# Optimization experiments

Hardware: AMD Instinct MI355X
Metric: run time of the kernel (lower is better)

## Reference

```python
import jax, jax.numpy as jnp
import numpy as np

K = 5          # kernel_size
PAD = 2        # padding
EPS = 1e-4     # epsilon (noise scale)
DEG = 4        # polynomial degree


def _unfold(x, k, pad):
    # PyTorch nn.Unfold ordering: feature index = c*k*k + i*k + j
    B, C, H, W = x.shape
    xp = jnp.pad(x, ((0, 0), (0, 0), (pad, pad), (pad, pad)))
    Ho = H + 2 * pad - k + 1
    Wo = W + 2 * pad - k + 1
    patches = jnp.stack(
        [xp[:, :, i:i + Ho, j:j + Wo] for i in range(k) for j in range(k)],
        axis=2,
    )  # [B, C, k*k, Ho, Wo]
    return patches.reshape(B, C * k * k, Ho * Wo), Ho, Wo


def setup_inputs() -> dict:
    key = jax.random.key(0)
    k1, k2, k3 = jax.random.split(key, 3)
    B, C, H = 4, 3, 96
    O, S = 32, 2
    y2 = jax.random.normal(k1, (B, C, H, H), dtype=jnp.float32)
    # kaiming_uniform_ on [O,C,k,k,S]: fan_in = C*k*k*S = 150
    bound = float(np.sqrt(6.0 / (C * K * K * S)))
    weights = jax.random.uniform(k2, (O, C, K, K, S), dtype=jnp.float32,
                                 minval=-bound, maxval=bound)
    L = H * H  # Ho*Wo with pad=2, k=5
    noise = jax.random.normal(k3, (B, C * K * K, L), dtype=jnp.float32)
    return {"y2": y2, "weights": weights, "noise": noise}


def reference(y2, weights, noise):
    O, C, k, _, S = weights.shape
    y, Ho, Wo = _unfold(y2, k, PAD)            # [B, n, L], n = C*k*k
    y = y + EPS * noise
    # normalize: torch.std default is unbiased (ddof=1) over feature dim
    std = jnp.std(y, axis=1, ddof=1)           # [B, L]
    y = y / std[:, None, :]

    X = weights.reshape(O, C * k * k, S)        # [O, n, S]
    # columns: [ones, X, X^2, ..., X^DEG]  -> P = 1 + S*DEG
    cols = [jnp.ones_like(X[:, :, :1])] + [X ** (i + 1) for i in range(DEG)]
    Xf = jnp.concatenate(cols, axis=2)          # [O, n, P]

    cov = jnp.einsum('onp,onq->opq', Xf, Xf)    # X^T X  [O, P, P]
    cov_inv = jnp.linalg.inv(cov)
    M = jnp.einsum('opq,onq->opn', cov_inv, Xf)
    W = jnp.einsum('opn,bnl->bopl', M, y)
    pred = jnp.einsum('onp,bopl->bonl', Xf, W)   # [B, O, n, L]

    err = jnp.mean((y[:, None, :, :] - pred) ** 2, axis=2)  # [B, O, L]
    err = err.reshape(err.shape[0], err.shape[1], Ho, Wo)

    e1 = np.exp(-1.0)
    A = (jnp.exp(-err) - e1) / (1.0 - e1)
    return A - 0.5
```

## Files before the change

### kernel.cpp

```cpp
#include <hip/hip_runtime.h>
#include <hip/hip_bf16.h>
#include <math.h>


typedef __attribute__((ext_vector_type(8))) short bf16x8;
typedef __attribute__((ext_vector_type(4))) float f32x4;
typedef __attribute__((ext_vector_type(4))) int i32x4;

#define TRI(p, q) ((p) * ((p) + 1) / 2 + (q))

__global__ __launch_bounds__(96) void srn_setup(const float* __restrict__ Wt,
                                                __hip_bfloat16* __restrict__ Gb) {
  const int o = blockIdx.x;
  __shared__ double Xf[96][9];
  __shared__ double Cm[9][9];
  __shared__ double Rf[45];
  __shared__ double scs[9];
  const int tid = threadIdx.x;
  if (tid < 75) {
    double x0 = (double)Wt[o * 150 + tid * 2 + 0];
    double x1 = (double)Wt[o * 150 + tid * 2 + 1];
    Xf[tid][0] = 1.0;
    double p = x0;
    Xf[tid][1] = p; p *= x0; Xf[tid][2] = p; p *= x0; Xf[tid][3] = p; p *= x0; Xf[tid][4] = p;
    p = x1;
    Xf[tid][5] = p; p *= x1; Xf[tid][6] = p; p *= x1; Xf[tid][7] = p; p *= x1; Xf[tid][8] = p;
  }
  __syncthreads();
  if (tid < 81) {
    const int p = tid / 9, q = tid - (tid / 9) * 9;
    double s = 0.0;
#pragma unroll
    for (int n = 0; n < 75; n++) s += Xf[n][p] * Xf[n][q];
    Cm[p][q] = s;
  }
  __syncthreads();
  if (tid == 0) {
    double sc[9];
#pragma unroll
    for (int p = 0; p < 9; p++) sc[p] = 1.0 / sqrt(Cm[p][p]);
    double A[45];
#pragma unroll
    for (int p = 0; p < 9; p++)
#pragma unroll
      for (int q = 0; q <= p; q++) A[TRI(p, q)] = Cm[p][q] * sc[p] * sc[q];
#pragma unroll
    for (int p = 0; p < 9; p++) {
      double s = A[TRI(p, p)];
#pragma unroll
      for (int i = 0; i < p; i++) s -= A[TRI(p, i)] * A[TRI(p, i)];
      const double rp = sqrt(s);
      A[TRI(p, p)] = rp;
      const double ir = 1.0 / rp;
#pragma unroll
      for (int r = p + 1; r < 9; r++) {
        double t = A[TRI(r, p)];
#pragma unroll
        for (int i = 0; i < p; i++) t -= A[TRI(r, i)] * A[TRI(p, i)];
        A[TRI(r, p)] = t * ir;
      }
    }
#pragma unroll
    for (int k = 0; k < 45; k++) Rf[k] = A[k];
#pragma unroll
    for (int p = 0; p < 9; p++) Rf[TRI(p, p)] = 1.0 / A[TRI(p, p)];
#pragma unroll
    for (int p = 0; p < 9; p++) scs[p] = sc[p];
  }
  __syncthreads();
  if (tid < 96) {
    double z[9];
    if (tid < 75) {
#pragma unroll
      for (int p = 0; p < 9; p++) {
        double s = scs[p] * Xf[tid][p];
#pragma unroll
        for (int i = 0; i < p; i++) s -= Rf[TRI(p, i)] * z[i];
        z[p] = s * Rf[TRI(p, p)];
      }
    } else {
#pragma unroll
      for (int p = 0; p < 9; p++) z[p] = 0.0;
    }
    const int t = o >> 1;
    const int ch = tid >> 5;
    const int g4r = (tid >> 3) & 3;
    const int j = tid & 7;
    const int base = ((t * 3 + ch) << 9) + ((o & 1) << 6) + (g4r << 7) + j;
#pragma unroll
    for (int p = 1; p < 9; p++)
      Gb[base + ((p - 1) << 3)] = __float2bfloat16((float)z[p]);
  }
}

__global__ __launch_bounds__(512, 2) void srn_main(const float* __restrict__ y2,
                                                   const __hip_bfloat16* __restrict__ Gbh,
                                                   float* __restrict__ out) {
  __shared__ __attribute__((aligned(16))) short Gs[24576];
  __shared__ int tab[96];

  const int tid = threadIdx.x;

  if (tid < 96) {
    const int c = (tid * 41) >> 10;
    const int r = tid - c * 25;
    const int di = (r * 52) >> 8;
    const int dj = r - di * 5;
    tab[tid] = (di << 20) | (dj << 16) | (c * 9216 + di * 96 + dj);
  }

  {
    const i32x4* gsrc = (const i32x4*)Gbh;
    i32x4* gdst = (i32x4*)Gs;
#pragma unroll
    for (int k = 0; k < 6; k++) gdst[k * 512 + tid] = gsrc[k * 512 + tid];
  }
  __syncthreads();

  const int lane = tid & 63;
  const int wv = tid >> 6;
  const int m16 = lane & 15, g4 = lane >> 4;
  const int tau2 = blockIdx.x * 8 + wv;
  const int b = tau2 / 576;
  const int rem = tau2 - b * 576;
  const int h = rem / 6;
  const int w0 = (rem - h * 6) * 16;
  const int w = w0 + m16;
  const int l = h * 96 + w;

  i32x4 e[6];
  const i32x4* tb = (const i32x4*)tab;
#pragma unroll
  for (int ch = 0; ch < 3; ch++) {
    e[ch * 2 + 0] = tb[ch * 8 + g4 * 2 + 0];
    e[ch * 2 + 1] = tb[ch * 8 + g4 * 2 + 1];
  }

  const float* yb = y2 + b * 27648;
  const bool fast = ((unsigned)(h - 2) < 92u) && (w0 >= 16) && (w0 <= 64);
  const int live1 = 11 - g4 * 8;
  float vv[24];
  if (fast) {
    const float* yl = yb + (l - 194);
#pragma unroll
    for (int ch = 0; ch < 3; ch++)
#pragma unroll
      for (int j = 0; j < 8; j++) {
        const int ent = (j < 4) ? e[ch * 2][j] : e[ch * 2 + 1][j - 4];
        float v = 0.f;
        if (ch < 2 || j < live1) v = yl[ent & 0xFFFF];
        vv[ch * 8 + j] = v;
      }
  } else {
#pragma unroll
    for (int ch = 0; ch < 3; ch++)
#pragma unroll
      for (int j = 0; j < 8; j++) {
        const int ent = (j < 4) ? e[ch * 2][j] : e[ch * 2 + 1][j - 4];
        float v = 0.f;
        if (ch < 2 || j < live1) {
          const int di = ent >> 20, dj = (ent >> 16) & 15;
          const int off = ent & 0xFFFF;
          const int c9216 = off - di * 96 - dj;
          const int hh = h + di - 2, ww = w + dj - 2;
          const float m = (((unsigned)hh < 96u) && ((unsigned)ww < 96u)) ? 1.f : 0.f;
          v = yb[c9216 + min(max(hh, 0), 95) * 96 + min(max(ww, 0), 95)] * m;
        }
        vv[ch * 8 + j] = v;
      }
  }

  bf16x8 Bf[3];
  float up = 0.f, sp = 0.f;
#pragma unroll
  for (int ch = 0; ch < 3; ch++)
#pragma unroll
    for (int j = 0; j < 8; j++) {
      const __hip_bfloat16 hb = __float2bfloat16(vv[ch * 8 + j]);
      const float vr = __bfloat162float(hb);
      sp += vr;
      up = fmaf(vr, vr, up);
      Bf[ch][j] = *reinterpret_cast<const short*>(&hb);
    }
  up += __shfl_xor(up, 16); up += __shfl_xor(up, 32);
  sp += __shfl_xor(sp, 16); sp += __shfl_xor(sp, 32);

  const float qbase = sp * sp * (1.f / 75.f);
  const float var = (up - qbase) * (1.f / 74.f);
  const float cerr = 1.f / (75.f * var);
  const float e1 = 0.36787944117144233f;
  const float r1 = 1.f / (1.f - e1);
  const float c2 = e1 * r1 + 0.5f;

  const short* Ab = Gs + lane * 8;
  float* ob = out + b * 294912 + l;
  const f32x4 z = {0.f, 0.f, 0.f, 0.f};
#pragma unroll
  for (int t = 0; t < 16; t++) {
    const short* At = Ab + t * 1536;
    const bf16x8 A0 = *(const bf16x8*)(At);
    const bf16x8 A1 = *(const bf16x8*)(At + 512);
    const bf16x8 A2 = *(const bf16x8*)(At + 1024);
    f32x4 acc = z;
    acc = __builtin_amdgcn_mfma_f32_16x16x32_bf16(A0, Bf[0], acc, 0, 0, 0);
    acc = __builtin_amdgcn_mfma_f32_16x16x32_bf16(A1, Bf[1], acc, 0, 0, 0);
    acc = __builtin_amdgcn_mfma_f32_16x16x32_bf16(A2, Bf[2], acc, 0, 0, 0);
    float qp = acc[0] * acc[0];
    qp = fmaf(acc[1], acc[1], qp);
    qp = fmaf(acc[2], acc[2], qp);
    qp = fmaf(acc[3], acc[3], qp);
    qp += __shfl_xor(qp, 16);
    const float q = qp + qbase;
    const float err = (up - q) * cerr;
    const float a = fmaf(__expf(-err), r1, -c2);
    if ((g4 & 1) == 0) ob[(2 * t + (g4 >> 1)) * 9216] = a;
  }
}

extern "C" void kernel_launch(void* const* d_in, const int* in_sizes, int n_in,
                              void* d_out, int out_size, void* d_ws, size_t ws_size,
                              hipStream_t stream) {
  const float* y2 = (const float*)d_in[0];
  const float* Wt = (const float*)d_in[1];
  float* out = (float*)d_out;
  __hip_bfloat16* Gb = (__hip_bfloat16*)d_ws;

  srn_setup<<<32, 96, 0, stream>>>(Wt, Gb);
  srn_main<<<288, 512, 0, stream>>>(y2, Gb, out);
}
```

Baseline: 20.86 us.

## Fuse weight-regression setup into main kernel, recomputing Cholesky per block

Removes the separate setup kernel and the workspace round-trip. Every block of the main kernel now computes the 32 Gram matrices, their Cholesky factors and the projected bf16 operand itself, using 16-lane shuffle reductions, and writes the result straight into shared memory. This saves one kernel launch and the dependent global write/read. In exchange, each of the 288 blocks repeats the double-precision setup work, and register pressure rises because of 45-element double arrays per thread.

```diff
diff --git a/kernel.cpp b/kernel.cpp
--- a/kernel.cpp
+++ b/kernel.cpp
@@ -9,94 +9,11 @@
 
 #define TRI(p, q) ((p) * ((p) + 1) / 2 + (q))
 
-__global__ __launch_bounds__(96) void srn_setup(const float* __restrict__ Wt,
-                                                __hip_bfloat16* __restrict__ Gb) {
-  const int o = blockIdx.x;
-  __shared__ double Xf[96][9];
-  __shared__ double Cm[9][9];
-  __shared__ double Rf[45];
-  __shared__ double scs[9];
-  const int tid = threadIdx.x;
-  if (tid < 75) {
-    double x0 = (double)Wt[o * 150 + tid * 2 + 0];
-    double x1 = (double)Wt[o * 150 + tid * 2 + 1];
-    Xf[tid][0] = 1.0;
-    double p = x0;
-    Xf[tid][1] = p; p *= x0; Xf[tid][2] = p; p *= x0; Xf[tid][3] = p; p *= x0; Xf[tid][4] = p;
-    p = x1;
-    Xf[tid][5] = p; p *= x1; Xf[tid][6] = p; p *= x1; Xf[tid][7] = p; p *= x1; Xf[tid][8] = p;
-  }
-  __syncthreads();
-  if (tid < 81) {
-    const int p = tid / 9, q = tid - (tid / 9) * 9;
-    double s = 0.0;
-#pragma unroll
-    for (int n = 0; n < 75; n++) s += Xf[n][p] * Xf[n][q];
-    Cm[p][q] = s;
-  }
-  __syncthreads();
-  if (tid == 0) {
-    double sc[9];
-#pragma unroll
-    for (int p = 0; p < 9; p++) sc[p] = 1.0 / sqrt(Cm[p][p]);
-    double A[45];
-#pragma unroll
-    for (int p = 0; p < 9; p++)
-#pragma unroll
-      for (int q = 0; q <= p; q++) A[TRI(p, q)] = Cm[p][q] * sc[p] * sc[q];
-#pragma unroll
-    for (int p = 0; p < 9; p++) {
-      double s = A[TRI(p, p)];
-#pragma unroll
-      for (int i = 0; i < p; i++) s -= A[TRI(p, i)] * A[TRI(p, i)];
-      const double rp = sqrt(s);
-      A[TRI(p, p)] = rp;
-      const double ir = 1.0 / rp;
-#pragma unroll
-      for (int r = p + 1; r < 9; r++) {
-        double t = A[TRI(r, p)];
-#pragma unroll
-        for (int i = 0; i < p; i++) t -= A[TRI(r, i)] * A[TRI(p, i)];
-        A[TRI(r, p)] = t * ir;
-      }
-    }
-#pragma unroll
-    for (int k = 0; k < 45; k++) Rf[k] = A[k];
-#pragma unroll
-    for (int p = 0; p < 9; p++) Rf[TRI(p, p)] = 1.0 / A[TRI(p, p)];
-#pragma unroll
-    for (int p = 0; p < 9; p++) scs[p] = sc[p];
-  }
-  __syncthreads();
-  if (tid < 96) {
-    double z[9];
-    if (tid < 75) {
-#pragma unroll
-      for (int p = 0; p < 9; p++) {
-        double s = scs[p] * Xf[tid][p];
-#pragma unroll
-        for (int i = 0; i < p; i++) s -= Rf[TRI(p, i)] * z[i];
-        z[p] = s * Rf[TRI(p, p)];
-      }
-    } else {
-#pragma unroll
-      for (int p = 0; p < 9; p++) z[p] = 0.0;
-    }
-    const int t = o >> 1;
-    const int ch = tid >> 5;
-    const int g4r = (tid >> 3) & 3;
-    const int j = tid & 7;
-    const int base = ((t * 3 + ch) << 9) + ((o & 1) << 6) + (g4r << 7) + j;
-#pragma unroll
-    for (int p = 1; p < 9; p++)
-      Gb[base + ((p - 1) << 3)] = __float2bfloat16((float)z[p]);
-  }
-}
-
-__global__ __launch_bounds__(512, 2) void srn_main(const float* __restrict__ y2,
-                                                   const __hip_bfloat16* __restrict__ Gbh,
-                                                   float* __restrict__ out) {
+__global__ __launch_bounds__(512, 2) void srn_fused(const float* __restrict__ y2,
+                                                    const float* __restrict__ Wt,
+                                                    float* __restrict__ out) {
   __shared__ __attribute__((aligned(16))) short Gs[24576];
+  __shared__ double RfL[32][54];
   __shared__ int tab[96];
 
   const int tid = threadIdx.x;
@@ -109,11 +26,97 @@
     tab[tid] = (di << 20) | (dj << 16) | (c * 9216 + di * 96 + dj);
   }
 
-  {
-    const i32x4* gsrc = (const i32x4*)Gbh;
-    i32x4* gdst = (i32x4*)Gs;
-#pragma unroll
-    for (int k = 0; k < 6; k++) gdst[k * 512 + tid] = gsrc[k * 512 + tid];
+  const int og = tid >> 4;
+  const int oj = tid & 15;
+
+  double cv[45];
+#pragma unroll
+  for (int i = 0; i < 45; i++) cv[i] = 0.0;
+#pragma unroll
+  for (int r = 0; r < 5; r++) {
+    const int n = oj + 16 * r;
+    if (n < 75) {
+      const double x0 = (double)Wt[og * 150 + 2 * n];
+      const double x1 = (double)Wt[og * 150 + 2 * n + 1];
+      double xf[9];
+      xf[0] = 1.0;
+      xf[1] = x0; xf[2] = x0 * x0; xf[3] = xf[2] * x0; xf[4] = xf[2] * xf[2];
+      xf[5] = x1; xf[6] = x1 * x1; xf[7] = xf[6] * x1; xf[8] = xf[6] * xf[6];
+      int idx = 0;
+#pragma unroll
+      for (int p = 0; p < 9; p++)
+#pragma unroll
+        for (int q = 0; q <= p; q++, idx++) cv[idx] = fma(xf[p], xf[q], cv[idx]);
+    }
+  }
+#pragma unroll
+  for (int m = 1; m < 16; m <<= 1)
+#pragma unroll
+    for (int i = 0; i < 45; i++) cv[i] += __shfl_xor(cv[i], m);
+
+  if (oj == 0) {
+    double sc[9];
+#pragma unroll
+    for (int p = 0; p < 9; p++) sc[p] = 1.0 / sqrt(cv[TRI(p, p)]);
+    double A[45];
+#pragma unroll
+    for (int p = 0; p < 9; p++)
+#pragma unroll
+      for (int q = 0; q <= p; q++) A[TRI(p, q)] = cv[TRI(p, q)] * sc[p] * sc[q];
+#pragma unroll
+    for (int p = 0; p < 9; p++) {
+      double s = A[TRI(p, p)];
+#pragma unroll
+      for (int i = 0; i < p; i++) s -= A[TRI(p, i)] * A[TRI(p, i)];
+      const double rp = sqrt(s);
+      A[TRI(p, p)] = rp;
+      const double ir = 1.0 / rp;
+#pragma unroll
+      for (int r = p + 1; r < 9; r++) {
+        double t = A[TRI(r, p)];
+#pragma unroll
+        for (int i = 0; i < p; i++) t -= A[TRI(r, i)] * A[TRI(p, i)];
+        A[TRI(r, p)] = t * ir;
+      }
+    }
+#pragma unroll
+    for (int k = 0; k < 45; k++) RfL[og][k] = A[k];
+#pragma unroll
+    for (int p = 0; p < 9; p++) RfL[og][TRI(p, p)] = 1.0 / A[TRI(p, p)];
+#pragma unroll
+    for (int p = 0; p < 9; p++) RfL[og][45 + p] = sc[p];
+  }
+  __syncthreads();
+
+#pragma unroll
+  for (int k = 0; k < 6; k++) {
+    const int n = oj + 16 * k;
+    double z[9];
+    if (n < 75) {
+      const double x0 = (double)Wt[og * 150 + 2 * n];
+      const double x1 = (double)Wt[og * 150 + 2 * n + 1];
+      double xf[9];
+      xf[0] = 1.0;
+      xf[1] = x0; xf[2] = x0 * x0; xf[3] = xf[2] * x0; xf[4] = xf[2] * xf[2];
+      xf[5] = x1; xf[6] = x1 * x1; xf[7] = xf[6] * x1; xf[8] = xf[6] * xf[6];
+#pragma unroll
+      for (int p = 0; p < 9; p++) {
+        double s = RfL[og][45 + p] * xf[p];
+#pragma unroll
+        for (int i = 0; i < p; i++) s -= RfL[og][TRI(p, i)] * z[i];
+        z[p] = s * RfL[og][TRI(p, p)];
+      }
+    } else {
+#pragma unroll
+      for (int p = 0; p < 9; p++) z[p] = 0.0;
+    }
+    const int t = og >> 1, ch = n >> 5, g4r = (n >> 3) & 3, jj = n & 7;
+    const int base = ((t * 3 + ch) << 9) + ((og & 1) << 6) + (g4r << 7) + jj;
+#pragma unroll
+    for (int p = 1; p < 9; p++) {
+      const __hip_bfloat16 hb = __float2bfloat16((float)z[p]);
+      Gs[base + ((p - 1) << 3)] = *reinterpret_cast<const short*>(&hb);
+    }
   }
   __syncthreads();
 
@@ -194,14 +197,14 @@
 
   const short* Ab = Gs + lane * 8;
   float* ob = out + b * 294912 + l;
-  const f32x4 z = {0.f, 0.f, 0.f, 0.f};
+  const f32x4 z4 = {0.f, 0.f, 0.f, 0.f};
 #pragma unroll
   for (int t = 0; t < 16; t++) {
     const short* At = Ab + t * 1536;
     const bf16x8 A0 = *(const bf16x8*)(At);
     const bf16x8 A1 = *(const bf16x8*)(At + 512);
     const bf16x8 A2 = *(const bf16x8*)(At + 1024);
-    f32x4 acc = z;
+    f32x4 acc = z4;
     acc = __builtin_amdgcn_mfma_f32_16x16x32_bf16(A0, Bf[0], acc, 0, 0, 0);
     acc = __builtin_amdgcn_mfma_f32_16x16x32_bf16(A1, Bf[1], acc, 0, 0, 0);
     acc = __builtin_amdgcn_mfma_f32_16x16x32_bf16(A2, Bf[2], acc, 0, 0, 0);
@@ -223,8 +226,5 @@
   const float* y2 = (const float*)d_in[0];
   const float* Wt = (const float*)d_in[1];
   float* out = (float*)d_out;
-  __hip_bfloat16* Gb = (__hip_bfloat16*)d_ws;
-
-  srn_setup<<<32, 96, 0, stream>>>(Wt, Gb);
-  srn_main<<<288, 512, 0, stream>>>(y2, Gb, out);
+  srn_fused<<<288, 512, 0, stream>>>(y2, Wt, out);
 }
```

Measured after the change: 75.32 us. 261% more time.
